# Performance work log

Hardware: AMD Instinct MI355X
Metric: run time of the kernel (lower is better)

## Reference

```python
import jax, jax.numpy as jnp
import numpy as np

H = 128      # hidden_dim
D = 129      # input_dim = 128 fused + 1 intent
SEQ = 12     # decode steps
OUT = 2      # trajectory point (x, y)


def setup_inputs() -> dict:
    key = jax.random.key(0)
    ks = jax.random.split(key, 16)
    B = 131072
    s = 0.05
    f32 = jnp.float32
    return {
        "fused_features": jax.random.normal(ks[0], (B, 128), f32),
        "intent_prob": jax.random.uniform(ks[1], (B, 1), f32),
        # init_hidden: Linear(D, 4H) -> h0/c0 for 2 layers
        "W_init": (jax.random.normal(ks[2], (4 * H, D), f32) * s),
        "b_init": (jax.random.normal(ks[3], (4 * H,), f32) * s),
        # LSTM layer 0 (input D), PyTorch gate order i, f, g, o
        "W_ih_l0": (jax.random.normal(ks[4], (4 * H, D), f32) * s),
        "W_hh_l0": (jax.random.normal(ks[5], (4 * H, H), f32) * s),
        "b_ih_l0": (jax.random.normal(ks[6], (4 * H,), f32) * s),
        "b_hh_l0": (jax.random.normal(ks[7], (4 * H,), f32) * s),
        # LSTM layer 1 (input H)
        "W_ih_l1": (jax.random.normal(ks[8], (4 * H, H), f32) * s),
        "W_hh_l1": (jax.random.normal(ks[9], (4 * H, H), f32) * s),
        "b_ih_l1": (jax.random.normal(ks[10], (4 * H,), f32) * s),
        "b_hh_l1": (jax.random.normal(ks[11], (4 * H,), f32) * s),
        # output head: Linear(H, OUT)
        "W_out": (jax.random.normal(ks[12], (OUT, H), f32) * s),
        "b_out": (jax.random.normal(ks[13], (OUT,), f32) * s),
    }


def _lstm_cell(pre, h, c, W_hh):
    # pre already contains x @ W_ih.T + b_ih + b_hh
    g = pre + h @ W_hh.T                      # [B, 4H]
    i, f, gg, o = jnp.split(g, 4, axis=1)     # PyTorch gate order i,f,g,o
    c_new = jax.nn.sigmoid(f) * c + jax.nn.sigmoid(i) * jnp.tanh(gg)
    h_new = jax.nn.sigmoid(o) * jnp.tanh(c_new)
    return h_new, c_new


def reference(fused_features, intent_prob, W_init, b_init,
              W_ih_l0, W_hh_l0, b_ih_l0, b_hh_l0,
              W_ih_l1, W_hh_l1, b_ih_l1, b_hh_l1,
              W_out, b_out):
    x = jnp.concatenate([fused_features, intent_prob], axis=1)   # [B, 129]
    B = x.shape[0]
    init = x @ W_init.T + b_init                                 # [B, 4H]
    # Faithful to torch: flat row-major reshape of [B, 2H] -> (2, B, H)
    h0 = init[:, : 2 * H].reshape(2, B, H)
    c0 = init[:, 2 * H :].reshape(2, B, H)

    # decoder input is the SAME features every step -> precompute input gates once
    pre0 = x @ W_ih_l0.T + b_ih_l0 + b_hh_l0                      # [B, 4H]

    def step(carry, _):
        h1, c1, h2, c2 = carry
        h1, c1 = _lstm_cell(pre0, h1, c1, W_hh_l0)
        pre1 = h1 @ W_ih_l1.T + b_ih_l1 + b_hh_l1
        h2, c2 = _lstm_cell(pre1, h2, c2, W_hh_l1)
        out = h2 @ W_out.T + b_out                                # [B, 2]
        return (h1, c1, h2, c2), out

    carry0 = (h0[0], c0[0], h0[1], c0[1])
    _, outs = jax.lax.scan(step, carry0, None, length=SEQ)        # [SEQ, B, 2]
    return jnp.transpose(outs, (1, 0, 2))                         # [B, SEQ, 2]
```

## Files before the change

### kernel.cpp

```cpp
#include <hip/hip_runtime.h>

#define SEQ 12

typedef __attribute__((ext_vector_type(8))) short bf16x8;
typedef __attribute__((ext_vector_type(4))) float f32x4;
typedef __attribute__((ext_vector_type(4))) unsigned short us4;

__device__ __forceinline__ unsigned short f2bf(float x) {
    unsigned u = __builtin_bit_cast(unsigned, x);
    u += 0x7fffu + ((u >> 16) & 1u);
    return (unsigned short)(u >> 16);
}
__device__ __forceinline__ float bf2f(unsigned short h) {
    unsigned u = ((unsigned)h) << 16;
    return __builtin_bit_cast(float, u);
}
__device__ __forceinline__ float sigf(float x) {
    return __builtin_amdgcn_rcpf(1.0f + __builtin_amdgcn_exp2f(-1.4426950408889634f * x));
}
__device__ __forceinline__ float tanhf_(float x) {
    return 1.0f - 2.0f * __builtin_amdgcn_rcpf(1.0f + __builtin_amdgcn_exp2f(2.8853900817779268f * x));
}

__global__ void pack_w(const float* __restrict__ Winit, const float* __restrict__ Wihl0,
                       const float* __restrict__ Whhl0, const float* __restrict__ Wihl1,
                       const float* __restrict__ Whhl1, unsigned short* __restrict__ pk,
                       int ncopy) {
    int id = blockIdx.x * 256 + threadIdx.x;
    if (id >= 327680) return;
    float v;
    if (id < 131072) {
        int e = id & 65535;
        int c = e >> 9, r = e & 511;
        int lane = r >> 3, j = r & 7;
        int kk = c & 3, G = (c >> 2) & 3, w = c >> 4;
        int n = G * 128 + w * 16 + (lane & 15);
        int k = kk * 32 + (lane >> 4) * 8 + j;
        const float* W = (id >> 16) ? Winit : Wihl0;
        v = W[n * 129 + k];
    } else if (id < 196608) {
        int e = id - 131072;
        int c = e >> 9, r = e & 511;
        int lane = r >> 3, j = r & 7;
        int kk = c & 3, G = (c >> 2) & 3, w = c >> 4;
        int n = G * 128 + w * 16 + (lane & 15);
        int k = kk * 32 + (lane >> 4) * 8 + j;
        v = Whhl0[n * 128 + k];
    } else {
        int e = id - 196608;
        int c = e >> 9, r = e & 511;
        int lane = r >> 3, j = r & 7;
        int kk = c & 7, G = (c >> 3) & 3, w = c >> 5;
        int n = G * 128 + w * 16 + (lane & 15);
        int k = kk * 32 + (lane >> 4) * 8 + j;
        v = (k < 128) ? Wihl1[n * 128 + k] : Whhl1[n * 128 + (k - 128)];
    }
    unsigned short hv = f2bf(v);
    for (int cpy = 0; cpy < ncopy; ++cpy) pk[cpy * 327680 + id] = hv;
}

#define LOAD_A(hb, kkl) do { _Pragma("unroll") \
    for (int mt = 0; mt < 4; ++mt) \
        a[mt] = *(const bf16x8*)&(hb)[(mt * 16 + nq) * 128 + ((((kkl) * 4 + quad) ^ nq) << 3)]; \
    } while (0)
#define LOAD_B(slot, base, KK, kk) do { _Pragma("unroll") \
    for (int G = 0; G < 4; ++G) \
        bb[slot][G] = *(const bf16x8*)&(base)[((w * 4 + G) * (KK) + (kk)) * 512 + lane * 8]; \
    } while (0)
#define MFMA_G(slot) do { _Pragma("unroll") \
    for (int mt = 0; mt < 4; ++mt) { _Pragma("unroll") \
        for (int G = 0; G < 4; ++G) \
            acc[mt][G] = __builtin_amdgcn_mfma_f32_16x16x32_bf16(a[mt], bb[slot][G], acc[mt][G], 0, 0, 0); } \
    } while (0)

__global__ __launch_bounds__(512) __attribute__((amdgpu_waves_per_eu(2, 2)))
void traj_main(const float* __restrict__ fused, const float* __restrict__ intent,
               const float* __restrict__ binit,
               const float* __restrict__ Winit, const float* __restrict__ Wihl0,
               const float* __restrict__ bihl0, const float* __restrict__ bhhl0,
               const float* __restrict__ bihl1, const float* __restrict__ bhhl1,
               const float* __restrict__ Wout, const float* __restrict__ bout,
               const unsigned short* __restrict__ pk,
               float* __restrict__ out, int Bsz) {
    __shared__ __align__(16) unsigned char s_u[32768];
    unsigned short* s_x  = (unsigned short*)s_u;
    unsigned short* s_xi = (unsigned short*)(s_u + 16384);
    unsigned short* s_c1 = (unsigned short*)s_u;
    unsigned short* s_c2 = (unsigned short*)(s_u + 16384);
    __shared__ __align__(16) float s_pre[4 * 512 * 4];
    __shared__ __align__(16) unsigned short s_h1[2][64 * 128];
    __shared__ __align__(16) unsigned short s_h2[2][64 * 128];
    __shared__ float s_wo[256];
    __shared__ float s_out[64 * 24];

    const int tid = threadIdx.x;
    const int lane = tid & 63;
    const int w = tid >> 6;
    const int nq = lane & 15;
    const int quad = lane >> 4;
    const int m0 = blockIdx.x * 64;
    const int Bh = Bsz >> 1;

    const unsigned short* pkPRE = pk;
    const unsigned short* pkINI = pk + 65536;
    const unsigned short* pkL0  = pk + 131072;
    const unsigned short* pkL1  = pk + 196608;

    if (tid < 256) s_wo[tid] = Wout[tid];
    const float bo2 = bout[(tid >> 2) & 1];

    float bpre[4], bl1[4], wcp[4], wci[4], bini[4];
#pragma unroll
    for (int G = 0; G < 4; ++G) {
        int n = G * 128 + w * 16 + nq;
        bpre[G] = bihl0[n] + bhhl0[n];
        bl1[G]  = bihl1[n] + bhhl1[n];
        wcp[G]  = Wihl0[n * 129 + 128];
        wci[G]  = Winit[n * 129 + 128];
        bini[G] = binit[n];
    }

#pragma unroll
    for (int it = 0; it < 8; ++it) {
        int f = it * 512 + tid;
        int row = f >> 5, fc = f & 31;
        int g = (row < 64) ? (m0 + row)
                           : ((row < 96) ? ((m0 >> 1) + (row - 64))
                                         : (Bh + (m0 >> 1) + (row - 96)));
        f32x4 v = *(const f32x4*)(fused + g * 128 + fc * 4);
        us4 u;
#pragma unroll
        for (int j = 0; j < 4; ++j) u[j] = f2bf(v[j]);
        int m = row & 63;
        int cp = (fc >> 1) ^ (m & 15);
        unsigned short* buf = (row < 64) ? s_x : s_xi;
        *(us4*)&buf[m * 128 + cp * 8 + (fc & 1) * 4] = u;
    }
    __syncthreads();

    {
        f32x4 acc2[4][4];
#pragma unroll
        for (int mt = 0; mt < 4; ++mt)
#pragma unroll
            for (int G = 0; G < 4; ++G)
                acc2[mt][G] = (f32x4){0.f, 0.f, 0.f, 0.f};
#pragma unroll
        for (int kk = 0; kk < 4; ++kk) {
            bf16x8 a2[4], b2[4];
#pragma unroll
            for (int mt = 0; mt < 4; ++mt)
                a2[mt] = *(const bf16x8*)&s_xi[(mt * 16 + nq) * 128 + (((kk * 4 + quad) ^ nq) << 3)];
#pragma unroll
            for (int G = 0; G < 4; ++G)
                b2[G] = *(const bf16x8*)&pkINI[((w * 4 + G) * 4 + kk) * 512 + lane * 8];
#pragma unroll
            for (int mt = 0; mt < 4; ++mt)
#pragma unroll
                for (int G = 0; G < 4; ++G)
                    acc2[mt][G] = __builtin_amdgcn_mfma_f32_16x16x32_bf16(a2[mt], b2[G], acc2[mt][G], 0, 0, 0);
        }
#pragma unroll
        for (int mt = 0; mt < 4; ++mt)
#pragma unroll
            for (int r = 0; r < 4; ++r) {
                int ml = mt * 16 + quad * 4 + r;
                int grow = (mt < 2) ? ((m0 >> 1) + ml) : (Bh + (m0 >> 1) + (ml - 32));
                float iv2 = intent[grow];
#pragma unroll
                for (int G = 0; G < 4; ++G)
                    acc2[mt][G][r] += bini[G] + iv2 * wci[G];
            }
        int kq = w * 16 + nq, kc = kq >> 3, klo = kq & 7;
#pragma unroll
        for (int mt = 0; mt < 4; ++mt)
#pragma unroll
            for (int r = 0; r < 4; ++r) {
                int ri = mt * 16 + quad * 4 + r;
                int layer = mt >> 1;
                int ril = ri & 31;
#pragma unroll
                for (int G = 0; G < 4; ++G) {
                    int ml = 2 * ril + (G & 1);
                    unsigned short hv = f2bf(acc2[mt][G][r]);
                    if (G < 2) {
                        unsigned short* hb = layer ? s_h2[0] : s_h1[0];
                        hb[ml * 128 + ((kc ^ (ml & 15)) << 3) + klo] = hv;
                    } else {
                        unsigned short* cb = layer ? s_h2[1] : s_h1[1];
                        cb[ml * 128 + kq] = hv;
                    }
                }
            }
    }

    f32x4 pre0[3][4], pre3[4];
#pragma unroll
    for (int G = 0; G < 4; ++G) {
        pre3[G] = (f32x4){0.f, 0.f, 0.f, 0.f};
#pragma unroll
        for (int mt = 0; mt < 3; ++mt)
            pre0[mt][G] = (f32x4){0.f, 0.f, 0.f, 0.f};
    }
#pragma unroll
    for (int kk = 0; kk < 4; ++kk) {
        bf16x8 av[4], bv[4];
#pragma unroll
        for (int mt = 0; mt < 4; ++mt)
            av[mt] = *(const bf16x8*)&s_x[(mt * 16 + nq) * 128 + (((kk * 4 + quad) ^ nq) << 3)];
#pragma unroll
        for (int G = 0; G < 4; ++G)
            bv[G] = *(const bf16x8*)&pkPRE[((w * 4 + G) * 4 + kk) * 512 + lane * 8];
#pragma unroll
        for (int mt = 0; mt < 4; ++mt)
#pragma unroll
            for (int G = 0; G < 4; ++G) {
                f32x4& pd = (mt < 3) ? pre0[mt][G] : pre3[G];
                pd = __builtin_amdgcn_mfma_f32_16x16x32_bf16(av[mt], bv[G], pd, 0, 0, 0);
            }
    }
#pragma unroll
    for (int mt = 0; mt < 4; ++mt)
#pragma unroll
        for (int r = 0; r < 4; ++r) {
            int ml = mt * 16 + quad * 4 + r;
            float iv = intent[m0 + ml];
#pragma unroll
            for (int G = 0; G < 4; ++G) {
                f32x4& pd = (mt < 3) ? pre0[mt][G] : pre3[G];
                pd[r] += bpre[G] + iv * wcp[G];
            }
        }
    __syncthreads();

#pragma unroll
    for (int G = 0; G < 4; ++G)
        *(f32x4*)&s_pre[G * 2048 + tid * 4] = pre3[G];
    {
        int kq = w * 16 + nq;
#pragma unroll
        for (int mt = 0; mt < 4; ++mt)
#pragma unroll
            for (int r = 0; r < 4; ++r) {
                int ml = mt * 16 + quad * 4 + r;
                s_c1[mt * 2048 + tid * 4 + r] = s_h1[1][ml * 128 + kq];
                s_c2[mt * 2048 + tid * 4 + r] = s_h2[1][ml * 128 + kq];
            }
    }
    __syncthreads();

    bf16x8 bb[2][4];
    LOAD_B(0, pkL0, 4, 0);
    LOAD_B(1, pkL0, 4, 1);

#pragma unroll 1
    for (int s = 0; s < SEQ; ++s) {
        const int p = s & 1;
        const unsigned short* h1r = s_h1[p];
        unsigned short*       h1w = s_h1[1 - p];
        const unsigned short* h2r = s_h2[p];
        unsigned short*       h2w = s_h2[1 - p];

        f32x4 acc[4][4];
        bf16x8 a[4];
#pragma unroll
        for (int mt = 0; mt < 3; ++mt)
#pragma unroll
            for (int G = 0; G < 4; ++G) acc[mt][G] = pre0[mt][G];
#pragma unroll
        for (int G = 0; G < 4; ++G)
            acc[3][G] = *(const f32x4*)&s_pre[G * 2048 + tid * 4];
        LOAD_A(h1r, 0); MFMA_G(0); LOAD_B(0, pkL0, 4, 2);
        LOAD_A(h1r, 1); MFMA_G(1); LOAD_B(1, pkL0, 4, 3);
        LOAD_A(h1r, 2); MFMA_G(0); LOAD_B(0, pkL1, 8, 0);
        LOAD_A(h1r, 3); MFMA_G(1); LOAD_B(1, pkL1, 8, 1);
#pragma unroll
        for (int mt = 0; mt < 4; ++mt) {
            us4 ch = *(const us4*)&s_c1[mt * 2048 + tid * 4];
#pragma unroll
            for (int r = 0; r < 4; ++r) {
                float iv = acc[mt][0][r], fv = acc[mt][1][r], gv = acc[mt][2][r], ov = acc[mt][3][r];
                float cn = sigf(fv) * bf2f(ch[r]) + sigf(iv) * tanhf_(gv);
                float hn = sigf(ov) * tanhf_(cn);
                ch[r] = f2bf(cn);
                int ml = mt * 16 + quad * 4 + r;
                h1w[ml * 128 + ((((w * 2) + (nq >> 3)) ^ (quad * 4 + r)) << 3) + (nq & 7)] = f2bf(hn);
            }
            *(us4*)&s_c1[mt * 2048 + tid * 4] = ch;
        }
        __syncthreads();
#pragma unroll
        for (int mt = 0; mt < 4; ++mt)
#pragma unroll
            for (int G = 0; G < 4; ++G)
                acc[mt][G] = (f32x4){bl1[G], bl1[G], bl1[G], bl1[G]};
        LOAD_A(h1w, 0); MFMA_G(0); LOAD_B(0, pkL1, 8, 2);
        LOAD_A(h1w, 1); MFMA_G(1); LOAD_B(1, pkL1, 8, 3);
        LOAD_A(h1w, 2); MFMA_G(0); LOAD_B(0, pkL1, 8, 4);
        LOAD_A(h1w, 3); MFMA_G(1); LOAD_B(1, pkL1, 8, 5);
        LOAD_A(h2r, 0); MFMA_G(0); LOAD_B(0, pkL1, 8, 6);
        LOAD_A(h2r, 1); MFMA_G(1); LOAD_B(1, pkL1, 8, 7);
        LOAD_A(h2r, 2); MFMA_G(0); LOAD_B(0, pkL0, 4, 0);
        LOAD_A(h2r, 3); MFMA_G(1); LOAD_B(1, pkL0, 4, 1);
#pragma unroll
        for (int mt = 0; mt < 4; ++mt) {
            us4 ch = *(const us4*)&s_c2[mt * 2048 + tid * 4];
#pragma unroll
            for (int r = 0; r < 4; ++r) {
                float iv = acc[mt][0][r], fv = acc[mt][1][r], gv = acc[mt][2][r], ov = acc[mt][3][r];
                float cn = sigf(fv) * bf2f(ch[r]) + sigf(iv) * tanhf_(gv);
                float hn = sigf(ov) * tanhf_(cn);
                ch[r] = f2bf(cn);
                int ml = mt * 16 + quad * 4 + r;
                h2w[ml * 128 + ((((w * 2) + (nq >> 3)) ^ (quad * 4 + r)) << 3) + (nq & 7)] = f2bf(hn);
            }
            *(us4*)&s_c2[mt * 2048 + tid * 4] = ch;
        }
        __syncthreads();
        {
            int ml = tid >> 3;
            int kc = tid & 3;
            const float* wr = s_wo + ((tid >> 2) & 1) * 128;
            int mx = ml & 15;
            float sum = 0.f;
#pragma unroll
            for (int c4 = 0; c4 < 4; ++c4) {
                int c = kc * 4 + c4;
                bf16x8 hv = *(const bf16x8*)&h2w[ml * 128 + ((c ^ mx) << 3)];
                int k0 = c << 3;
#pragma unroll
                for (int j = 0; j < 8; ++j)
                    sum += bf2f((unsigned short)hv[j]) * wr[k0 + j];
            }
            sum += __shfl_xor(sum, 1);
            sum += __shfl_xor(sum, 2);
            if (kc == 0) s_out[ml * 24 + s * 2 + ((tid >> 2) & 1)] = sum + bo2;
        }
    }
    __syncthreads();
    for (int i = tid; i < 1536; i += 512) out[m0 * 24 + i] = s_out[i];
}

extern "C" void kernel_launch(void* const* d_in, const int* in_sizes, int n_in,
                              void* d_out, int out_size, void* d_ws, size_t ws_size,
                              hipStream_t stream) {
    const float* fused  = (const float*)d_in[0];
    const float* intent = (const float*)d_in[1];
    const float* Winit  = (const float*)d_in[2];
    const float* binit  = (const float*)d_in[3];
    const float* Wihl0  = (const float*)d_in[4];
    const float* Whhl0  = (const float*)d_in[5];
    const float* bihl0  = (const float*)d_in[6];
    const float* bhhl0  = (const float*)d_in[7];
    const float* Wihl1  = (const float*)d_in[8];
    const float* Whhl1  = (const float*)d_in[9];
    const float* bihl1  = (const float*)d_in[10];
    const float* bhhl1  = (const float*)d_in[11];
    const float* Wout   = (const float*)d_in[12];
    const float* bout   = (const float*)d_in[13];
    int Bsz = in_sizes[0] / 128;

    unsigned short* pkw = (unsigned short*)d_ws;
    pack_w<<<1280, 256, 0, stream>>>(Winit, Wihl0, Whhl0, Wihl1, Whhl1, pkw, 1);
    traj_main<<<Bsz / 64, 512, 0, stream>>>(fused, intent, binit, Winit, Wihl0, bihl0,
                                            bhhl0, bihl1, bhhl1, Wout, bout, pkw,
                                            (float*)d_out, Bsz);
}
```

Baseline: 1.880 ms.

## Recompute layer-0 input projection each step instead of caching pre-gates

Drops the precomputed layer-0 input-gate tile (48 accumulator registers plus a 32KB shared buffer). Each decode step now recomputes x @ W_ih_l0 with extra MFMAs from a persistent bf16 copy of x in shared memory, seeded with bias plus intent times weight. The shared-memory layout is reorganised so x stays resident while the c-state buffers are kept separate. This cuts register pressure and LDS use at the cost of 16 extra MFMA groups and more B-weight loads per step.

```diff
diff --git a/kernel.cpp b/kernel.cpp
--- a/kernel.cpp
+++ b/kernel.cpp
@@ -82,12 +82,11 @@
                const float* __restrict__ Wout, const float* __restrict__ bout,
                const unsigned short* __restrict__ pk,
                float* __restrict__ out, int Bsz) {
-    __shared__ __align__(16) unsigned char s_u[32768];
-    unsigned short* s_x  = (unsigned short*)s_u;
-    unsigned short* s_xi = (unsigned short*)(s_u + 16384);
+    __shared__ __align__(16) unsigned short s_x[64 * 128];
+    __shared__ __align__(16) unsigned char  s_u[16384];
+    unsigned short* s_xi = (unsigned short*)s_u;
     unsigned short* s_c1 = (unsigned short*)s_u;
-    unsigned short* s_c2 = (unsigned short*)(s_u + 16384);
-    __shared__ __align__(16) float s_pre[4 * 512 * 4];
+    __shared__ __align__(16) unsigned short s_c2[4 * 512 * 4];
     __shared__ __align__(16) unsigned short s_h1[2][64 * 128];
     __shared__ __align__(16) unsigned short s_h2[2][64 * 128];
     __shared__ float s_wo[256];
@@ -119,6 +118,12 @@
         wci[G]  = Winit[n * 129 + 128];
         bini[G] = binit[n];
     }
+    f32x4 ivv[4];
+#pragma unroll
+    for (int mt = 0; mt < 4; ++mt)
+#pragma unroll
+        for (int r = 0; r < 4; ++r)
+            ivv[mt][r] = intent[m0 + mt * 16 + quad * 4 + r];
 
 #pragma unroll
     for (int it = 0; it < 8; ++it) {
@@ -193,49 +198,8 @@
                 }
             }
     }
-
-    f32x4 pre0[3][4], pre3[4];
-#pragma unroll
-    for (int G = 0; G < 4; ++G) {
-        pre3[G] = (f32x4){0.f, 0.f, 0.f, 0.f};
-#pragma unroll
-        for (int mt = 0; mt < 3; ++mt)
-            pre0[mt][G] = (f32x4){0.f, 0.f, 0.f, 0.f};
-    }
-#pragma unroll
-    for (int kk = 0; kk < 4; ++kk) {
-        bf16x8 av[4], bv[4];
-#pragma unroll
-        for (int mt = 0; mt < 4; ++mt)
-            av[mt] = *(const bf16x8*)&s_x[(mt * 16 + nq) * 128 + (((kk * 4 + quad) ^ nq) << 3)];
-#pragma unroll
-        for (int G = 0; G < 4; ++G)
-            bv[G] = *(const bf16x8*)&pkPRE[((w * 4 + G) * 4 + kk) * 512 + lane * 8];
-#pragma unroll
-        for (int mt = 0; mt < 4; ++mt)
-#pragma unroll
-            for (int G = 0; G < 4; ++G) {
-                f32x4& pd = (mt < 3) ? pre0[mt][G] : pre3[G];
-                pd = __builtin_amdgcn_mfma_f32_16x16x32_bf16(av[mt], bv[G], pd, 0, 0, 0);
-            }
-    }
-#pragma unroll
-    for (int mt = 0; mt < 4; ++mt)
-#pragma unroll
-        for (int r = 0; r < 4; ++r) {
-            int ml = mt * 16 + quad * 4 + r;
-            float iv = intent[m0 + ml];
-#pragma unroll
-            for (int G = 0; G < 4; ++G) {
-                f32x4& pd = (mt < 3) ? pre0[mt][G] : pre3[G];
-                pd[r] += bpre[G] + iv * wcp[G];
-            }
-        }
     __syncthreads();
 
-#pragma unroll
-    for (int G = 0; G < 4; ++G)
-        *(f32x4*)&s_pre[G * 2048 + tid * 4] = pre3[G];
     {
         int kq = w * 16 + nq;
 #pragma unroll
@@ -250,8 +214,8 @@
     __syncthreads();
 
     bf16x8 bb[2][4];
-    LOAD_B(0, pkL0, 4, 0);
-    LOAD_B(1, pkL0, 4, 1);
+    LOAD_B(0, pkPRE, 4, 0);
+    LOAD_B(1, pkPRE, 4, 1);
 
 #pragma unroll 1
     for (int s = 0; s < SEQ; ++s) {
@@ -264,12 +228,16 @@
         f32x4 acc[4][4];
         bf16x8 a[4];
 #pragma unroll
-        for (int mt = 0; mt < 3; ++mt)
-#pragma unroll
-            for (int G = 0; G < 4; ++G) acc[mt][G] = pre0[mt][G];
-#pragma unroll
-        for (int G = 0; G < 4; ++G)
-            acc[3][G] = *(const f32x4*)&s_pre[G * 2048 + tid * 4];
+        for (int mt = 0; mt < 4; ++mt)
+#pragma unroll
+            for (int G = 0; G < 4; ++G)
+#pragma unroll
+                for (int rr = 0; rr < 4; ++rr)
+                    acc[mt][G][rr] = bpre[G] + ivv[mt][rr] * wcp[G];
+        LOAD_A(s_x, 0); MFMA_G(0); LOAD_B(0, pkPRE, 4, 2);
+        LOAD_A(s_x, 1); MFMA_G(1); LOAD_B(1, pkPRE, 4, 3);
+        LOAD_A(s_x, 2); MFMA_G(0); LOAD_B(0, pkL0, 4, 0);
+        LOAD_A(s_x, 3); MFMA_G(1); LOAD_B(1, pkL0, 4, 1);
         LOAD_A(h1r, 0); MFMA_G(0); LOAD_B(0, pkL0, 4, 2);
         LOAD_A(h1r, 1); MFMA_G(1); LOAD_B(1, pkL0, 4, 3);
         LOAD_A(h1r, 2); MFMA_G(0); LOAD_B(0, pkL1, 8, 0);
@@ -300,8 +268,8 @@
         LOAD_A(h1w, 3); MFMA_G(1); LOAD_B(1, pkL1, 8, 5);
         LOAD_A(h2r, 0); MFMA_G(0); LOAD_B(0, pkL1, 8, 6);
         LOAD_A(h2r, 1); MFMA_G(1); LOAD_B(1, pkL1, 8, 7);
-        LOAD_A(h2r, 2); MFMA_G(0); LOAD_B(0, pkL0, 4, 0);
-        LOAD_A(h2r, 3); MFMA_G(1); LOAD_B(1, pkL0, 4, 1);
+        LOAD_A(h2r, 2); MFMA_G(0); LOAD_B(0, pkPRE, 4, 0);
+        LOAD_A(h2r, 3); MFMA_G(1); LOAD_B(1, pkPRE, 4, 1);
 #pragma unroll
         for (int mt = 0; mt < 4; ++mt) {
             us4 ch = *(const us4*)&s_c2[mt * 2048 + tid * 4];
```

Result: slower. 2.509 ms (+33.5%).
